# Kernel optimization log

Measured on AMD Instinct MI355X. Metric: run time of the kernel, lower is better.

Reference implementation:

```python
import jax, jax.numpy as jnp
import numpy as np
from jax import lax

DT = 0.001          # integration step
SCALE = 0.2         # hopf_input_scale
NUM_STEPS = 5       # Euler sub-steps per sequence position
MU = 1.0            # Hopf limit-cycle radius^2


def hopf_layer(h, omega):
    """Hopf oscillator bank driven by h: [B, T, U]; omega: [U] (rad/s).
    For each sequence position, run NUM_STEPS Euler steps of
      dx = (mu - (x^2+y^2)) x - omega*y + scale*u
      dy = (mu - (x^2+y^2)) y + omega*x
    carrying (x, y) state across positions. Returns per-position states
    (z_real, z_imag), each [B, T, U]."""

    def per_timestep(state, u):  # u: [B, U]
        def euler(c, _):
            x, y = c
            r2 = x * x + y * y
            nx = x + DT * ((MU - r2) * x - omega * y + SCALE * u)
            ny = y + DT * ((MU - r2) * y + omega * x)
            return (nx, ny), None
        state, _ = lax.scan(euler, state, None, length=NUM_STEPS)
        return state, state

    B, T, U = h.shape
    z0 = (jnp.zeros((B, U), h.dtype), jnp.zeros((B, U), h.dtype))
    _, (xs, ys) = lax.scan(per_timestep, z0, jnp.swapaxes(h, 0, 1))  # [T,B,U]
    return jnp.swapaxes(xs, 0, 1), jnp.swapaxes(ys, 0, 1)


def setup_inputs() -> dict:
    key = jax.random.key(0)
    ks = jax.random.split(key, 12)
    B, T = 128, 1024
    V, E, U, P, C = 50000, 100, 100, 20, 2
    two_pi = 2.0 * np.pi
    return {
        "x": jax.random.randint(ks[0], (B, T), 0, V),
        "emb": jax.random.normal(ks[1], (V, E), jnp.float32) * 0.05,
        "omega1": jax.random.uniform(ks[2], (U,), jnp.float32, two_pi * 1.0, two_pi * 15.0),
        "omega2": jax.random.uniform(ks[3], (U,), jnp.float32, two_pi * 1.0, two_pi * 15.0),
        "w1": jax.random.normal(ks[4], (2 * U, U), jnp.float32) * 0.07,
        "b1": jnp.zeros((U,), jnp.float32),
        "w2": jax.random.normal(ks[5], (2 * U, U), jnp.float32) * 0.07,
        "b2": jnp.zeros((U,), jnp.float32),
        "wp": jax.random.normal(ks[6], (U, P), jnp.float32) * 0.1,
        "bp": jnp.zeros((P,), jnp.float32),
        "wh": jax.random.normal(ks[7], (P, C), jnp.float32) * 0.2,
        "bh": jnp.zeros((C,), jnp.float32),
    }


def reference(x, emb, omega1, omega2, w1, b1, w2, b2, wp, bp, wh, bh):
    h0 = emb[x]                                   # [B, T, E]
    z1r, z1i = hopf_layer(h0, omega1)             # [B, T, U] each
    h1 = jax.nn.relu(jnp.concatenate([z1r, z1i], axis=2) @ w1 + b1)
    z2r, z2i = hopf_layer(h1, omega2)
    h2 = jax.nn.relu(jnp.concatenate([z2r, z2i], axis=2) @ w2 + b2)
    last = h2[:, -1, :]                           # many-to-one: last timestep
    h3 = jnp.tanh(last @ wp + bp)                 # [B, P]
    return h3 @ wh + bh                           # [B, C]
```

## Files before the change

### kernel.cpp

```cpp
#include <hip/hip_runtime.h>
#include <cmath>

namespace {
constexpr int T = 1024, BATCH = 128, U = 100, E = 100, P = 20, C = 2;
constexpr int TC = 64, NC = 16;
constexpr float DT = 0.001f, SCALE = 0.2f, MU = 1.0f;

constexpr uint32_t WROW = 464u, ZROW = 464u, HROW = 200u, EROW = 200u;
constexpr uint32_t WLB = 0u;
constexpr uint32_t ZBB = 46400u, ZBUF = 64u * ZROW;
constexpr uint32_t HBB = ZBB + 2u * ZBUF;
constexpr uint32_t HBUF = 64u * HROW;
constexpr uint32_t EBB = HBB + 2u * HBUF;
constexpr uint32_t EBUF = 64u * EROW;
constexpr uint32_t ARENA = EBB + 2u * EBUF;

typedef _Float16 f16x8 __attribute__((ext_vector_type(8)));
typedef float f32x4 __attribute__((ext_vector_type(4)));
typedef _Float16 h2_t __attribute__((ext_vector_type(2)));

__device__ __forceinline__ void eul5(float& xx, float& yy, float dom, float ax) {
    constexpr float c0 = 1.0f + DT * MU;
#pragma unroll
    for (int s = 0; s < 5; ++s) {
        float r2 = fmaf(yy, yy, xx * xx);
        float sc = fmaf(-DT, r2, c0);
        float nx = fmaf(xx, sc, fmaf(-dom, yy, ax));
        float ny = fmaf(yy, sc, dom * xx);
        xx = nx; yy = ny;
    }
}

__launch_bounds__(512, 1)
__global__ void donn_kernel(const int* __restrict__ xg,
                            const float* __restrict__ emb,
                            const float* __restrict__ omega1,
                            const float* __restrict__ omega2,
                            const float* __restrict__ w1,
                            const float* __restrict__ b1,
                            const float* __restrict__ w2,
                            const float* __restrict__ b2,
                            const float* __restrict__ wp,
                            const float* __restrict__ bp,
                            const float* __restrict__ wh,
                            const float* __restrict__ bh,
                            float* __restrict__ out)
{
    const int b = blockIdx.x;
    const int tid = threadIdx.x;

    __shared__ __align__(16) char smem[ARENA];
    __shared__ int xs[2][TC];
    __shared__ float zf2[2][104];
    __shared__ float pb[2][104];
    __shared__ float h2s[104];
    __shared__ float h3s[32];

    float x1 = 0.f, y1 = 0.f, x2 = 0.f, y2 = 0.f;
    float dom1 = 0.f, dom2 = 0.f;
    int jc = 0, j2c = 0;
    int mw = 0, lane = 0;
    float b1r[7];
    uint32_t brow[7];
    int urow[25], ucol[25];

    if (tid < 128) {
        jc = (tid < U) ? tid : (U - 1);
        dom1 = DT * omega1[jc];
    } else if (tid < 256) {
        const int j2 = tid - 128;
        j2c = (j2 < U) ? j2 : (U - 1);
        dom2 = DT * omega2[j2c];
    } else {
        mw = (tid >> 6) - 4;
        lane = tid & 63;
#pragma unroll
        for (int n = 0; n < 7; ++n) {
            int j = n * 16 + (lane & 15);
            int jj = (j < U) ? j : (U - 1);
            b1r[n] = b1[jj];
            brow[n] = WLB + (uint32_t)jj * WROW + 16u * (uint32_t)(lane >> 4);
        }
        const int e = tid - 256;
#pragma unroll
        for (int i = 0; i < 25; ++i) {
            int idx = i * 256 + e;
            int row = idx / 100;
            urow[i] = row;
            ucol[i] = idx - 100 * row;
        }
    }

    for (int idx = tid; idx < 200 * 100; idx += 512) {
        int k = idx / 100, j = idx - 100 * k;
        float v = w1[k * U + j];
        int kp = (k < U) ? (2 * k) : (2 * (k - U) + 1);
        *(_Float16*)(smem + WLB + (uint32_t)j * WROW + 2 * kp) = (_Float16)v;
    }
    for (int idx = tid; idx < 228 * 16; idx += 512) {
        int row = idx >> 4, wd = idx & 15;
        uint32_t base;
        if (row < 100) base = WLB + (uint32_t)row * WROW;
        else {
            int zr = row - 100;
            base = ZBB + (uint32_t)(zr >> 6) * ZBUF + (uint32_t)(zr & 63) * ZROW;
        }
        *(float*)(smem + base + 400u + 4u * (uint32_t)wd) = 0.f;
    }
    for (int idx = tid; idx < TC * E; idx += 512) {
        int row = idx / 100, col = idx - 100 * row;
        int tok = xg[b * T + row];
        *(_Float16*)(smem + EBB + (uint32_t)row * EROW + 2 * col) = (_Float16)emb[tok * E + col];
    }
    if (tid < TC) xs[1][tid] = xg[b * T + TC + tid];
    __syncthreads();

    for (int p = 0; p <= NC + 1; ++p) {
        if (tid < 128) {
            if (p < NC) {
                const uint32_t q = (uint32_t)(p & 1);
                const char* eb = smem + EBB + q * EBUF;
                char* zb = smem + ZBB + q * ZBUF;
                const bool act = tid < U;
#pragma unroll 8
                for (int tl = 0; tl < TC; ++tl) {
                    float u = (float)(*(const _Float16*)(eb + (uint32_t)tl * EROW + 2 * jc));
                    eul5(x1, y1, dom1, (DT * SCALE) * u);
                    if (act) {
                        h2_t zz; zz[0] = (_Float16)x1; zz[1] = (_Float16)y1;
                        *(h2_t*)(zb + (uint32_t)tl * ZROW + 4u * (uint32_t)tid) = zz;
                    }
                }
            }
        } else if (tid < 256) {
            if (p >= 2) {
                const uint32_t q = (uint32_t)(p & 1);
                const char* hb = smem + HBB + q * HBUF;
#pragma unroll 8
                for (int tl = 0; tl < TC; ++tl) {
                    float hv = (float)(*(const _Float16*)(hb + (uint32_t)tl * HROW + 2 * j2c));
                    eul5(x2, y2, dom2, (DT * SCALE) * hv);
                }
            }
            if (p + 2 < NC && tid - 128 < TC)
                xs[p & 1][tid - 128] = xg[b * T + (p + 2) * TC + (tid - 128)];
        } else {
            float er[25];
            const bool edo = (p + 1 < NC);
            if (edo) {
                const int q2 = (p + 1) & 1;
#pragma unroll
                for (int i = 0; i < 25; ++i) {
                    int tok = xs[q2][urow[i]];
                    er[i] = emb[tok * E + ucol[i]];
                }
            }
            if (p >= 1 && p <= NC) {
                const uint32_t qm = (uint32_t)((p - 1) & 1);
                const char* zb = smem + ZBB + qm * ZBUF;
                const uint32_t arow = (uint32_t)(mw * 16 + (lane & 15)) * ZROW
                                      + 16u * (uint32_t)(lane >> 4);
                f32x4 acc[7];
#pragma unroll
                for (int n = 0; n < 7; ++n) acc[n] = (f32x4)0.f;
#pragma unroll
                for (int ks = 0; ks < 7; ++ks) {
                    f16x8 af = *(const f16x8*)(zb + arow + 64u * ks);
#pragma unroll
                    for (int n = 0; n < 7; ++n) {
                        f16x8 bf = *(const f16x8*)(smem + brow[n] + 64u * ks);
                        acc[n] = __builtin_amdgcn_mfma_f32_16x16x32_f16(af, bf, acc[n], 0, 0, 0);
                    }
                }
                char* hb = smem + HBB + qm * HBUF;
#pragma unroll
                for (int n = 0; n < 7; ++n) {
                    const int j = n * 16 + (lane & 15);
                    if (j < U) {
#pragma unroll
                        for (int r = 0; r < 4; ++r) {
                            int t = mw * 16 + (lane >> 4) * 4 + r;
                            float h = fmaxf(acc[n][r] + b1r[n], 0.f);
                            *(_Float16*)(hb + (uint32_t)t * HROW + 2 * j) = (_Float16)h;
                        }
                    }
                }
            }
            if (edo) {
                const int q2 = (p + 1) & 1;
                char* eb = smem + EBB + (uint32_t)q2 * EBUF;
#pragma unroll
                for (int i = 0; i < 25; ++i)
                    *(_Float16*)(eb + (uint32_t)urow[i] * EROW + 2 * ucol[i]) = (_Float16)er[i];
            }
        }
        __syncthreads();
    }

    if (tid >= 128 && tid < 256) {
        const int j = tid - 128;
        if (j < U) { zf2[0][j] = x2; zf2[1][j] = y2; }
    }
    __syncthreads();

    if (tid >= 256 && tid < 456) {
        const int e = tid - 256;
        const int h = e / 100, jq = e - 100 * (e / 100);
        float acc2 = 0.f;
#pragma unroll 4
        for (int kk = 0; kk < 100; ++kk)
            acc2 = fmaf(zf2[h][kk], w2[(100 * h + kk) * U + jq], acc2);
        pb[h][jq] = acc2;
    }
    __syncthreads();

    if (tid < U) h2s[tid] = fmaxf(pb[0][tid] + pb[1][tid] + b2[tid], 0.f);
    __syncthreads();

    if (tid < P) {
        float acc = bp[tid];
#pragma unroll 4
        for (int j = 0; j < U; ++j) acc = fmaf(h2s[j], wp[j * P + tid], acc);
        h3s[tid] = tanhf(acc);
    }
    __syncthreads();

    if (tid < C) {
        float acc = bh[tid];
#pragma unroll
        for (int pp = 0; pp < P; ++pp) acc = fmaf(h3s[pp], wh[pp * C + tid], acc);
        out[b * C + tid] = acc;
    }
}
}

extern "C" void kernel_launch(void* const* d_in, const int* in_sizes, int n_in,
                              void* d_out, int out_size, void* d_ws, size_t ws_size,
                              hipStream_t stream) {
    const int* xi        = (const int*)d_in[0];
    const float* emb     = (const float*)d_in[1];
    const float* omega1  = (const float*)d_in[2];
    const float* omega2  = (const float*)d_in[3];
    const float* w1      = (const float*)d_in[4];
    const float* b1      = (const float*)d_in[5];
    const float* w2      = (const float*)d_in[6];
    const float* b2      = (const float*)d_in[7];
    const float* wp      = (const float*)d_in[8];
    const float* bp      = (const float*)d_in[9];
    const float* wh      = (const float*)d_in[10];
    const float* bh      = (const float*)d_in[11];
    float* out           = (float*)d_out;

    hipLaunchKernelGGL(donn_kernel, dim3(BATCH), dim3(512), 0, stream,
                       xi, emb, omega1, omega2, w1, b1, w2, b2, wp, bp, wh, bh, out);
}
```

Before: 149.6 us.

## Merge oscillator layers into one warp group, async-load embeddings, register-cache W1

```diff
diff --git a/kernel.cpp b/kernel.cpp
--- a/kernel.cpp
+++ b/kernel.cpp
@@ -5,19 +5,20 @@
 constexpr int T = 1024, BATCH = 128, U = 100, E = 100, P = 20, C = 2;
 constexpr int TC = 64, NC = 16;
 constexpr float DT = 0.001f, SCALE = 0.2f, MU = 1.0f;
-
-constexpr uint32_t WROW = 464u, ZROW = 464u, HROW = 200u, EROW = 200u;
-constexpr uint32_t WLB = 0u;
-constexpr uint32_t ZBB = 46400u, ZBUF = 64u * ZROW;
-constexpr uint32_t HBB = ZBB + 2u * ZBUF;
-constexpr uint32_t HBUF = 64u * HROW;
-constexpr uint32_t EBB = HBB + 2u * HBUF;
-constexpr uint32_t EBUF = 64u * EROW;
-constexpr uint32_t ARENA = EBB + 2u * EBUF;
+constexpr float DTS = DT * SCALE;
+
+constexpr uint32_t WROW = 464u, ZROW = 464u, HROW = 200u;
+constexpr uint32_t EBUF = 25600u;
+constexpr uint32_t ZBB = 51200u, ZBUF = 29696u;
+constexpr uint32_t HBB = 110592u, HBUF = 12800u;
+constexpr uint32_t ARENA = 136192u;
 
 typedef _Float16 f16x8 __attribute__((ext_vector_type(8)));
 typedef float f32x4 __attribute__((ext_vector_type(4)));
 typedef _Float16 h2_t __attribute__((ext_vector_type(2)));
+
+#define AS1 __attribute__((address_space(1)))
+#define AS3 __attribute__((address_space(3)))
 
 __device__ __forceinline__ void eul5(float& xx, float& yy, float dom, float ax) {
     constexpr float c0 = 1.0f + DT * MU;
@@ -31,7 +32,7 @@
     }
 }
 
-__launch_bounds__(512, 1)
+__launch_bounds__(384, 2)
 __global__ void donn_kernel(const int* __restrict__ xg,
                             const float* __restrict__ emb,
                             const float* __restrict__ omega1,
@@ -58,153 +59,160 @@
 
     float x1 = 0.f, y1 = 0.f, x2 = 0.f, y2 = 0.f;
     float dom1 = 0.f, dom2 = 0.f;
-    int jc = 0, j2c = 0;
-    int mw = 0, lane = 0;
-    float b1r[7];
-    uint32_t brow[7];
-    int urow[25], ucol[25];
-
-    if (tid < 128) {
-        jc = (tid < U) ? tid : (U - 1);
-        dom1 = DT * omega1[jc];
-    } else if (tid < 256) {
-        const int j2 = tid - 128;
-        j2c = (j2 < U) ? j2 : (U - 1);
-        dom2 = DT * omega2[j2c];
+    int mh = 0, n0 = 0, lane = 0;
+    float b1r[4] = {0.f, 0.f, 0.f, 0.f};
+    f16x8 Bf[4][7];
+
+    const bool is_osc = (tid < 128);
+    if (is_osc) {
+        const int j = (tid < U) ? tid : (U - 1);
+        dom1 = DT * omega1[j];
+        dom2 = DT * omega2[j];
     } else {
-        mw = (tid >> 6) - 4;
+        const int mw = (tid >> 6) - 2;
         lane = tid & 63;
-#pragma unroll
-        for (int n = 0; n < 7; ++n) {
-            int j = n * 16 + (lane & 15);
+        mh = mw >> 1;
+        n0 = (mw & 1) * 4;
+    }
+
+    if (tid < TC) xs[0][tid] = xg[b * T + tid];
+    else if (tid < 2 * TC) xs[1][tid - TC] = xg[b * T + TC + (tid - TC)];
+    for (int idx = tid; idx < 200 * 100; idx += 384) {
+        int k = idx / 100, j = idx - 100 * k;
+        int kp = (k < U) ? (2 * k) : (2 * (k - U) + 1);
+        *(_Float16*)(smem + (uint32_t)j * WROW + 2 * kp) = (_Float16)w1[k * U + j];
+    }
+    for (int idx = tid; idx < 100 * 16; idx += 384) {
+        int row = idx >> 4, wd = idx & 15;
+        *(float*)(smem + (uint32_t)row * WROW + 400u + 4u * (uint32_t)wd) = 0.f;
+    }
+    for (int idx = tid; idx < 128 * 16; idx += 384) {
+        int zr = idx >> 4, wd = idx & 15;
+        uint32_t base = ZBB + (uint32_t)(zr >> 6) * ZBUF + (uint32_t)(zr & 63) * ZROW;
+        *(float*)(smem + base + 400u + 4u * (uint32_t)wd) = 0.f;
+    }
+    __syncthreads();
+
+    if (!is_osc) {
+#pragma unroll
+        for (int n = 0; n < 4; ++n) {
+            int j = (n0 + n) * 16 + (lane & 15);
             int jj = (j < U) ? j : (U - 1);
             b1r[n] = b1[jj];
-            brow[n] = WLB + (uint32_t)jj * WROW + 16u * (uint32_t)(lane >> 4);
+            uint32_t br = (uint32_t)jj * WROW + 16u * (uint32_t)(lane >> 4);
+#pragma unroll
+            for (int ks = 0; ks < 7; ++ks)
+                Bf[n][ks] = *(const f16x8*)(smem + br + 64u * ks);
         }
-        const int e = tid - 256;
-#pragma unroll
-        for (int i = 0; i < 25; ++i) {
-            int idx = i * 256 + e;
-            int row = idx / 100;
-            urow[i] = row;
-            ucol[i] = idx - 100 * row;
-        }
-    }
-
-    for (int idx = tid; idx < 200 * 100; idx += 512) {
-        int k = idx / 100, j = idx - 100 * k;
-        float v = w1[k * U + j];
-        int kp = (k < U) ? (2 * k) : (2 * (k - U) + 1);
-        *(_Float16*)(smem + WLB + (uint32_t)j * WROW + 2 * kp) = (_Float16)v;
-    }
-    for (int idx = tid; idx < 228 * 16; idx += 512) {
-        int row = idx >> 4, wd = idx & 15;
-        uint32_t base;
-        if (row < 100) base = WLB + (uint32_t)row * WROW;
-        else {
-            int zr = row - 100;
-            base = ZBB + (uint32_t)(zr >> 6) * ZBUF + (uint32_t)(zr & 63) * ZROW;
-        }
-        *(float*)(smem + base + 400u + 4u * (uint32_t)wd) = 0.f;
-    }
-    for (int idx = tid; idx < TC * E; idx += 512) {
-        int row = idx / 100, col = idx - 100 * row;
-        int tok = xg[b * T + row];
-        *(_Float16*)(smem + EBB + (uint32_t)row * EROW + 2 * col) = (_Float16)emb[tok * E + col];
-    }
-    if (tid < TC) xs[1][tid] = xg[b * T + TC + tid];
+    }
+    __syncthreads();
+
+    for (int idx = tid; idx < TC * E; idx += 384) {
+        int t = idx / 100, c = idx - 100 * t;
+        int tok = xs[0][t];
+        *(float*)(smem + (uint32_t)t * 400u + 4u * (uint32_t)c) = emb[tok * E + c];
+    }
     __syncthreads();
 
     for (int p = 0; p <= NC + 1; ++p) {
-        if (tid < 128) {
-            if (p < NC) {
-                const uint32_t q = (uint32_t)(p & 1);
-                const char* eb = smem + EBB + q * EBUF;
-                char* zb = smem + ZBB + q * ZBUF;
-                const bool act = tid < U;
-#pragma unroll 8
-                for (int tl = 0; tl < TC; ++tl) {
-                    float u = (float)(*(const _Float16*)(eb + (uint32_t)tl * EROW + 2 * jc));
-                    eul5(x1, y1, dom1, (DT * SCALE) * u);
-                    if (act) {
+        if (is_osc) {
+            if (tid < TC && p + 2 < NC)
+                xs[p & 1][tid] = xg[b * T + (p + 2) * TC + tid];
+            if (tid < U) {
+                const bool do1 = p < NC, do2 = p >= 2;
+                const float* eb = (const float*)(smem + (uint32_t)(p & 1) * EBUF);
+                const char* hb = smem + HBB + (uint32_t)(p & 1) * HBUF;
+                char* zb = smem + ZBB + (uint32_t)(p & 1) * ZBUF;
+                if (do1 && do2) {
+#pragma unroll 4
+                    for (int tl = 0; tl < TC; ++tl) {
+                        float u = eb[tl * 100 + tid];
+                        eul5(x1, y1, dom1, DTS * u);
                         h2_t zz; zz[0] = (_Float16)x1; zz[1] = (_Float16)y1;
                         *(h2_t*)(zb + (uint32_t)tl * ZROW + 4u * (uint32_t)tid) = zz;
+                        float hv = (float)(*(const _Float16*)(hb + (uint32_t)tl * HROW + 2u * (uint32_t)tid));
+                        eul5(x2, y2, dom2, DTS * hv);
+                    }
+                } else if (do1) {
+#pragma unroll 4
+                    for (int tl = 0; tl < TC; ++tl) {
+                        float u = eb[tl * 100 + tid];
+                        eul5(x1, y1, dom1, DTS * u);
+                        h2_t zz; zz[0] = (_Float16)x1; zz[1] = (_Float16)y1;
+                        *(h2_t*)(zb + (uint32_t)tl * ZROW + 4u * (uint32_t)tid) = zz;
+                    }
+                } else if (do2) {
+#pragma unroll 4
+                    for (int tl = 0; tl < TC; ++tl) {
+                        float hv = (float)(*(const _Float16*)(hb + (uint32_t)tl * HROW + 2u * (uint32_t)tid));
+                        eul5(x2, y2, dom2, DTS * hv);
                     }
                 }
             }
-        } else if (tid < 256) {
-            if (p >= 2) {
-                const uint32_t q = (uint32_t)(p & 1);
-                const char* hb = smem + HBB + q * HBUF;
-#pragma unroll 8
-                for (int tl = 0; tl < TC; ++tl) {
-                    float hv = (float)(*(const _Float16*)(hb + (uint32_t)tl * HROW + 2 * j2c));
-                    eul5(x2, y2, dom2, (DT * SCALE) * hv);
-                }
-            }
-            if (p + 2 < NC && tid - 128 < TC)
-                xs[p & 1][tid - 128] = xg[b * T + (p + 2) * TC + (tid - 128)];
         } else {
-            float er[25];
-            const bool edo = (p + 1 < NC);
-            if (edo) {
-                const int q2 = (p + 1) & 1;
+            const int mw = mh * 2 + (n0 >> 2);
+            if (p + 1 < NC) {
+                const uint32_t qe = (uint32_t)((p + 1) & 1);
 #pragma unroll
                 for (int i = 0; i < 25; ++i) {
-                    int tok = xs[q2][urow[i]];
-                    er[i] = emb[tok * E + ucol[i]];
+                    int f = (mw * 25 + i) * 64 + lane;
+                    int t = f / 100;
+                    int c = f - 100 * t;
+                    int tok = xs[qe][t];
+                    const float* g = emb + tok * E + c;
+                    char* l = smem + qe * EBUF + (uint32_t)(mw * 25 + i) * 256u;
+                    __builtin_amdgcn_global_load_lds((const AS1 void*)(const void*)g,
+                                                     (AS3 void*)(void*)l, 4, 0, 0);
                 }
             }
             if (p >= 1 && p <= NC) {
                 const uint32_t qm = (uint32_t)((p - 1) & 1);
                 const char* zb = smem + ZBB + qm * ZBUF;
-                const uint32_t arow = (uint32_t)(mw * 16 + (lane & 15)) * ZROW
-                                      + 16u * (uint32_t)(lane >> 4);
-                f32x4 acc[7];
-#pragma unroll
-                for (int n = 0; n < 7; ++n) acc[n] = (f32x4)0.f;
-#pragma unroll
-                for (int ks = 0; ks < 7; ++ks) {
-                    f16x8 af = *(const f16x8*)(zb + arow + 64u * ks);
-#pragma unroll
-                    for (int n = 0; n < 7; ++n) {
-                        f16x8 bf = *(const f16x8*)(smem + brow[n] + 64u * ks);
-                        acc[n] = __builtin_amdgcn_mfma_f32_16x16x32_f16(af, bf, acc[n], 0, 0, 0);
-                    }
+                char* hb = smem + HBB + qm * HBUF;
+                f32x4 acc[2][4];
+#pragma unroll
+                for (int mt = 0; mt < 2; ++mt)
+#pragma unroll
+                    for (int n = 0; n < 4; ++n) acc[mt][n] = (f32x4)0.f;
+#pragma unroll
+                for (int mt = 0; mt < 2; ++mt) {
+                    const uint32_t ar = (uint32_t)(mh * 32 + mt * 16 + (lane & 15)) * ZROW
+                                        + 16u * (uint32_t)(lane >> 4);
+                    f16x8 af[7];
+#pragma unroll
+                    for (int ks = 0; ks < 7; ++ks)
+                        af[ks] = *(const f16x8*)(zb + ar + 64u * ks);
+#pragma unroll
+                    for (int n = 0; n < 4; ++n)
+#pragma unroll
+                        for (int ks = 0; ks < 7; ++ks)
+                            acc[mt][n] = __builtin_amdgcn_mfma_f32_16x16x32_f16(
+                                af[ks], Bf[n][ks], acc[mt][n], 0, 0, 0);
                 }
-                char* hb = smem + HBB + qm * HBUF;
-#pragma unroll
-                for (int n = 0; n < 7; ++n) {
-                    const int j = n * 16 + (lane & 15);
-                    if (j < U) {
-#pragma unroll
-                        for (int r = 0; r < 4; ++r) {
-                            int t = mw * 16 + (lane >> 4) * 4 + r;
-                            float h = fmaxf(acc[n][r] + b1r[n], 0.f);
-                            *(_Float16*)(hb + (uint32_t)t * HROW + 2 * j) = (_Float16)h;
+#pragma unroll
+                for (int mt = 0; mt < 2; ++mt)
+#pragma unroll
+                    for (int n = 0; n < 4; ++n) {
+                        const int j = (n0 + n) * 16 + (lane & 15);
+                        if (j < U) {
+#pragma unroll
+                            for (int r = 0; r < 4; ++r) {
+                                int t = mh * 32 + mt * 16 + (lane >> 4) * 4 + r;
+                                float h = fmaxf(acc[mt][n][r] + b1r[n], 0.f);
+                                *(_Float16*)(hb + (uint32_t)t * HROW + 2u * (uint32_t)j) = (_Float16)h;
+                            }
                         }
                     }
-                }
-            }
-            if (edo) {
-                const int q2 = (p + 1) & 1;
-                char* eb = smem + EBB + (uint32_t)q2 * EBUF;
-#pragma unroll
-                for (int i = 0; i < 25; ++i)
-                    *(_Float16*)(eb + (uint32_t)urow[i] * EROW + 2 * ucol[i]) = (_Float16)er[i];
             }
         }
         __syncthreads();
     }
 
-    if (tid >= 128 && tid < 256) {
-        const int j = tid - 128;
-        if (j < U) { zf2[0][j] = x2; zf2[1][j] = y2; }
-    }
-    __syncthreads();
-
-    if (tid >= 256 && tid < 456) {
-        const int e = tid - 256;
+    if (tid < U) { zf2[0][tid] = x2; zf2[1][tid] = y2; }
+    __syncthreads();
+
+    if (tid >= 128 && tid < 328) {
+        const int e = tid - 128;
         const int h = e / 100, jq = e - 100 * (e / 100);
         float acc2 = 0.f;
 #pragma unroll 4
@@ -251,6 +259,6 @@
     const float* bh      = (const float*)d_in[11];
     float* out           = (float*)d_out;
 
-    hipLaunchKernelGGL(donn_kernel, dim3(BATCH), dim3(512), 0, stream,
+    hipLaunchKernelGGL(donn_kernel, dim3(BATCH), dim3(384), 0, stream,
                        xi, emb, omega1, omega2, w1, b1, w2, b2, wp, bp, wh, bh, out);
 }
```

Measured after the change: 201.9 us. +34.9%, slower.

## Transpose and swizzle E/H buffers for vectorized recurrence loads, retile MFMA

Applied to the files above, without the earlier changes.

```diff
diff --git a/kernel.cpp b/kernel.cpp
--- a/kernel.cpp
+++ b/kernel.cpp
@@ -5,17 +5,17 @@
 constexpr int T = 1024, BATCH = 128, U = 100, E = 100, P = 20, C = 2;
 constexpr int TC = 64, NC = 16;
 constexpr float DT = 0.001f, SCALE = 0.2f, MU = 1.0f;
-
-constexpr uint32_t WROW = 464u, ZROW = 464u, HROW = 200u, EROW = 200u;
+constexpr float DTS = DT * SCALE;
+
+constexpr uint32_t WROW = 464u, ZROW = 464u, EROW = 128u, HROW = 128u;
 constexpr uint32_t WLB = 0u;
-constexpr uint32_t ZBB = 46400u, ZBUF = 64u * ZROW;
-constexpr uint32_t HBB = ZBB + 2u * ZBUF;
-constexpr uint32_t HBUF = 64u * HROW;
-constexpr uint32_t EBB = HBB + 2u * HBUF;
-constexpr uint32_t EBUF = 64u * EROW;
-constexpr uint32_t ARENA = EBB + 2u * EBUF;
+constexpr uint32_t ZBB = 46400u, ZBUF = 29696u;
+constexpr uint32_t EBB = 105792u, EBUF = 12800u;
+constexpr uint32_t HBB = 131392u, HBUF = 12800u;
+constexpr uint32_t ARENA = 156992u;
 
 typedef _Float16 f16x8 __attribute__((ext_vector_type(8)));
+typedef _Float16 f16x4 __attribute__((ext_vector_type(4)));
 typedef float f32x4 __attribute__((ext_vector_type(4)));
 typedef _Float16 h2_t __attribute__((ext_vector_type(2)));
 
@@ -59,13 +59,14 @@
     float x1 = 0.f, y1 = 0.f, x2 = 0.f, y2 = 0.f;
     float dom1 = 0.f, dom2 = 0.f;
     int jc = 0, j2c = 0;
-    int mw = 0, lane = 0;
-    float b1r[7];
-    uint32_t brow[7];
-    int urow[25], ucol[25];
+    bool act1 = false;
+    int mw = 0, lane = 0, mh = 0, n0 = 0;
+    float b1r[4] = {0.f, 0.f, 0.f, 0.f};
+    uint32_t brow[4] = {0u, 0u, 0u, 0u};
 
     if (tid < 128) {
         jc = (tid < U) ? tid : (U - 1);
+        act1 = tid < U;
         dom1 = DT * omega1[jc];
     } else if (tid < 256) {
         const int j2 = tid - 128;
@@ -74,124 +75,160 @@
     } else {
         mw = (tid >> 6) - 4;
         lane = tid & 63;
-#pragma unroll
-        for (int n = 0; n < 7; ++n) {
-            int j = n * 16 + (lane & 15);
+        mh = mw >> 1;
+        n0 = (mw & 1) * 4;
+#pragma unroll
+        for (int n = 0; n < 4; ++n) {
+            int j = (n0 + n) * 16 + (lane & 15);
             int jj = (j < U) ? j : (U - 1);
             b1r[n] = b1[jj];
             brow[n] = WLB + (uint32_t)jj * WROW + 16u * (uint32_t)(lane >> 4);
         }
-        const int e = tid - 256;
-#pragma unroll
-        for (int i = 0; i < 25; ++i) {
-            int idx = i * 256 + e;
-            int row = idx / 100;
-            urow[i] = row;
-            ucol[i] = idx - 100 * row;
-        }
-    }
-
+    }
+
+    if (tid < TC) xs[0][tid] = xg[b * T + tid];
+    else if (tid < 2 * TC) xs[1][tid - TC] = xg[b * T + TC + (tid - TC)];
     for (int idx = tid; idx < 200 * 100; idx += 512) {
         int k = idx / 100, j = idx - 100 * k;
-        float v = w1[k * U + j];
         int kp = (k < U) ? (2 * k) : (2 * (k - U) + 1);
-        *(_Float16*)(smem + WLB + (uint32_t)j * WROW + 2 * kp) = (_Float16)v;
-    }
-    for (int idx = tid; idx < 228 * 16; idx += 512) {
+        *(_Float16*)(smem + WLB + (uint32_t)j * WROW + 2u * (uint32_t)kp) = (_Float16)w1[k * U + j];
+    }
+    for (int idx = tid; idx < 100 * 16; idx += 512) {
         int row = idx >> 4, wd = idx & 15;
-        uint32_t base;
-        if (row < 100) base = WLB + (uint32_t)row * WROW;
-        else {
-            int zr = row - 100;
-            base = ZBB + (uint32_t)(zr >> 6) * ZBUF + (uint32_t)(zr & 63) * ZROW;
-        }
+        *(float*)(smem + WLB + (uint32_t)row * WROW + 400u + 4u * (uint32_t)wd) = 0.f;
+    }
+    for (int idx = tid; idx < 128 * 16; idx += 512) {
+        int zr = idx >> 4, wd = idx & 15;
+        uint32_t base = ZBB + (uint32_t)(zr >> 6) * ZBUF + (uint32_t)(zr & 63) * ZROW;
         *(float*)(smem + base + 400u + 4u * (uint32_t)wd) = 0.f;
     }
-    for (int idx = tid; idx < TC * E; idx += 512) {
-        int row = idx / 100, col = idx - 100 * row;
-        int tok = xg[b * T + row];
-        *(_Float16*)(smem + EBB + (uint32_t)row * EROW + 2 * col) = (_Float16)emb[tok * E + col];
-    }
-    if (tid < TC) xs[1][tid] = xg[b * T + TC + tid];
+    __syncthreads();
+    for (int idx = tid; idx < 100 * TC; idx += 512) {
+        int j = idx >> 6, t = idx & 63;
+        int tok = xs[0][t];
+        uint32_t off = EBB + (uint32_t)j * EROW
+                     + (uint32_t)(((((t >> 3) ^ (j & 7))) << 4) + 2 * (t & 7));
+        *(_Float16*)(smem + off) = (_Float16)emb[tok * E + j];
+    }
     __syncthreads();
 
     for (int p = 0; p <= NC + 1; ++p) {
         if (tid < 128) {
+            if (tid < TC && p + 2 < NC)
+                xs[p & 1][tid] = xg[b * T + (p + 2) * TC + tid];
             if (p < NC) {
                 const uint32_t q = (uint32_t)(p & 1);
-                const char* eb = smem + EBB + q * EBUF;
-                char* zb = smem + ZBB + q * ZBUF;
-                const bool act = tid < U;
-#pragma unroll 8
-                for (int tl = 0; tl < TC; ++tl) {
-                    float u = (float)(*(const _Float16*)(eb + (uint32_t)tl * EROW + 2 * jc));
-                    eul5(x1, y1, dom1, (DT * SCALE) * u);
-                    if (act) {
-                        h2_t zz; zz[0] = (_Float16)x1; zz[1] = (_Float16)y1;
-                        *(h2_t*)(zb + (uint32_t)tl * ZROW + 4u * (uint32_t)tid) = zz;
+                const char* ebase = smem + EBB + q * EBUF + (uint32_t)jc * EROW;
+                char* zbase = smem + ZBB + q * ZBUF + 4u * (uint32_t)jc;
+                const int s = jc & 7;
+                f16x8 eA = *(const f16x8*)(ebase + ((0 ^ s) << 4));
+                for (int gg = 0; gg < 4; ++gg) {
+                    f16x8 eB = *(const f16x8*)(ebase + (((2 * gg + 1) ^ s) << 4));
+                    {
+                        char* zt = zbase + (uint32_t)(16 * gg) * ZROW;
+#pragma unroll
+                        for (int i = 0; i < 8; ++i) {
+                            eul5(x1, y1, dom1, DTS * (float)eA[i]);
+                            if (act1) {
+                                h2_t zz; zz[0] = (_Float16)x1; zz[1] = (_Float16)y1;
+                                *(h2_t*)(zt + (uint32_t)i * ZROW) = zz;
+                            }
+                        }
+                    }
+                    if (gg < 3) eA = *(const f16x8*)(ebase + (((2 * gg + 2) ^ s) << 4));
+                    {
+                        char* zt = zbase + (uint32_t)(16 * gg + 8) * ZROW;
+#pragma unroll
+                        for (int i = 0; i < 8; ++i) {
+                            eul5(x1, y1, dom1, DTS * (float)eB[i]);
+                            if (act1) {
+                                h2_t zz; zz[0] = (_Float16)x1; zz[1] = (_Float16)y1;
+                                *(h2_t*)(zt + (uint32_t)i * ZROW) = zz;
+                            }
+                        }
                     }
                 }
             }
         } else if (tid < 256) {
             if (p >= 2) {
                 const uint32_t q = (uint32_t)(p & 1);
-                const char* hb = smem + HBB + q * HBUF;
-#pragma unroll 8
-                for (int tl = 0; tl < TC; ++tl) {
-                    float hv = (float)(*(const _Float16*)(hb + (uint32_t)tl * HROW + 2 * j2c));
-                    eul5(x2, y2, dom2, (DT * SCALE) * hv);
-                }
-            }
-            if (p + 2 < NC && tid - 128 < TC)
-                xs[p & 1][tid - 128] = xg[b * T + (p + 2) * TC + (tid - 128)];
+                const char* hbase = smem + HBB + q * HBUF + (uint32_t)j2c * HROW;
+                const int s = j2c & 7;
+                f16x8 eA = *(const f16x8*)(hbase + ((0 ^ s) << 4));
+                for (int gg = 0; gg < 4; ++gg) {
+                    f16x8 eB = *(const f16x8*)(hbase + (((2 * gg + 1) ^ s) << 4));
+#pragma unroll
+                    for (int i = 0; i < 8; ++i)
+                        eul5(x2, y2, dom2, DTS * (float)eA[i]);
+                    if (gg < 3) eA = *(const f16x8*)(hbase + (((2 * gg + 2) ^ s) << 4));
+#pragma unroll
+                    for (int i = 0; i < 8; ++i)
+                        eul5(x2, y2, dom2, DTS * (float)eB[i]);
+                }
+            }
         } else {
             float er[25];
             const bool edo = (p + 1 < NC);
             if (edo) {
-                const int q2 = (p + 1) & 1;
-#pragma unroll
-                for (int i = 0; i < 25; ++i) {
-                    int tok = xs[q2][urow[i]];
-                    er[i] = emb[tok * E + ucol[i]];
-                }
+                const uint32_t qe = (uint32_t)((p + 1) & 1);
+                int tok = xs[qe][lane];
+                const float* ep = emb + (size_t)tok * E;
+#pragma unroll
+                for (int i = 0; i < 25; ++i) er[i] = ep[mw * 25 + i];
             }
             if (p >= 1 && p <= NC) {
                 const uint32_t qm = (uint32_t)((p - 1) & 1);
                 const char* zb = smem + ZBB + qm * ZBUF;
-                const uint32_t arow = (uint32_t)(mw * 16 + (lane & 15)) * ZROW
-                                      + 16u * (uint32_t)(lane >> 4);
-                f32x4 acc[7];
-#pragma unroll
-                for (int n = 0; n < 7; ++n) acc[n] = (f32x4)0.f;
-#pragma unroll
-                for (int ks = 0; ks < 7; ++ks) {
-                    f16x8 af = *(const f16x8*)(zb + arow + 64u * ks);
-#pragma unroll
-                    for (int n = 0; n < 7; ++n) {
-                        f16x8 bf = *(const f16x8*)(smem + brow[n] + 64u * ks);
-                        acc[n] = __builtin_amdgcn_mfma_f32_16x16x32_f16(af, bf, acc[n], 0, 0, 0);
+                f32x4 acc[2][4];
+#pragma unroll
+                for (int mt = 0; mt < 2; ++mt)
+#pragma unroll
+                    for (int n = 0; n < 4; ++n) acc[mt][n] = (f32x4)0.f;
+#pragma unroll
+                for (int mt = 0; mt < 2; ++mt) {
+                    const uint32_t ar = (uint32_t)(mh * 32 + mt * 16 + (lane & 15)) * ZROW
+                                        + 16u * (uint32_t)(lane >> 4);
+                    f16x8 af[7];
+#pragma unroll
+                    for (int ks = 0; ks < 7; ++ks)
+                        af[ks] = *(const f16x8*)(zb + ar + 64u * ks);
+#pragma unroll
+                    for (int n = 0; n < 4; ++n)
+#pragma unroll
+                        for (int ks = 0; ks < 7; ++ks) {
+                            f16x8 bf = *(const f16x8*)(smem + brow[n] + 64u * ks);
+                            acc[mt][n] = __builtin_amdgcn_mfma_f32_16x16x32_f16(
+                                af[ks], bf, acc[mt][n], 0, 0, 0);
+                        }
+                }
+                char* hb = smem + HBB + qm * HBUF;
+#pragma unroll
+                for (int mt = 0; mt < 2; ++mt)
+#pragma unroll
+                    for (int n = 0; n < 4; ++n) {
+                        const int j = (n0 + n) * 16 + (lane & 15);
+                        if (j < U) {
+                            const int t0v = mh * 32 + mt * 16 + (lane >> 4) * 4;
+                            f16x4 hv;
+#pragma unroll
+                            for (int r = 0; r < 4; ++r)
+                                hv[r] = (_Float16)fmaxf(acc[mt][n][r] + b1r[n], 0.f);
+                            uint32_t off = (uint32_t)j * HROW
+                                + (uint32_t)(((((t0v >> 3) ^ (j & 7))) << 4) + ((2 * t0v) & 15));
+                            *(f16x4*)(hb + off) = hv;
+                        }
                     }
-                }
-                char* hb = smem + HBB + qm * HBUF;
-#pragma unroll
-                for (int n = 0; n < 7; ++n) {
-                    const int j = n * 16 + (lane & 15);
-                    if (j < U) {
-#pragma unroll
-                        for (int r = 0; r < 4; ++r) {
-                            int t = mw * 16 + (lane >> 4) * 4 + r;
-                            float h = fmaxf(acc[n][r] + b1r[n], 0.f);
-                            *(_Float16*)(hb + (uint32_t)t * HROW + 2 * j) = (_Float16)h;
-                        }
-                    }
-                }
             }
             if (edo) {
-                const int q2 = (p + 1) & 1;
-                char* eb = smem + EBB + (uint32_t)q2 * EBUF;
-#pragma unroll
-                for (int i = 0; i < 25; ++i)
-                    *(_Float16*)(eb + (uint32_t)urow[i] * EROW + 2 * ucol[i]) = (_Float16)er[i];
+                const uint32_t qe = (uint32_t)((p + 1) & 1);
+                char* eb = smem + EBB + qe * EBUF;
+#pragma unroll
+                for (int i = 0; i < 25; ++i) {
+                    int jrow = mw * 25 + i;
+                    uint32_t off = (uint32_t)jrow * EROW
+                        + (uint32_t)(((((lane >> 3) ^ (jrow & 7))) << 4) + 2 * (lane & 7));
+                    *(_Float16*)(eb + off) = (_Float16)er[i];
+                }
             }
         }
         __syncthreads();
```

After: 127.9 us. 14.5% less time.
